# Performance work log

Measured on AMD Instinct MI355X. Metric: run time of the kernel, lower is better.

The kernel has to match this reference:

```python
import jax, jax.numpy as jnp
import numpy as np

N = 16384      # total points
B = 8          # point clouds in batch
PER = N // B   # points per cloud (batch ids sorted in blocks)
M = 4096       # sampled centers (ratio 0.25, strided sampler -> batch-aligned)
K = 64         # max_num_neighbors
R = 0.25       # ball-query radius
C_IN = 128
HID = 256
C_OUT = 256


def setup_inputs() -> dict:
    key = jax.random.key(0)
    k1, k2, k3, k4, k5 = jax.random.split(key, 5)
    x = jax.random.normal(k1, (N, C_IN), dtype=jnp.float32)
    pos = jax.random.uniform(k2, (N, 3), dtype=jnp.float32)  # unit cube
    batch = jnp.repeat(jnp.arange(B, dtype=jnp.int32), PER)  # sorted block batch ids
    lframes = jax.random.normal(k3, (N, 3, 3), dtype=jnp.float32)
    W1 = jax.random.normal(k4, (2 * C_IN + 3, HID), dtype=jnp.float32) * 0.05
    b1 = jnp.zeros((HID,), dtype=jnp.float32)
    W2 = jax.random.normal(k5, (HID, C_OUT), dtype=jnp.float32) * 0.05
    b2 = jnp.zeros((C_OUT,), dtype=jnp.float32)
    return {"x": x, "pos": pos, "batch": batch, "lframes": lframes,
            "W1": W1, "b1": b1, "W2": W2, "b2": b2}


def _ball_query(pos, batch, idx):
    """radius(pos, pos[idx], R, batch, batch[idx], max_num_neighbors=K).
    Returns fixed-size neighbor indices [M, K] + validity mask [M, K]."""
    pos_c = pos[idx]                                  # [M, 3]
    # squared distances via gemm trick (avoid [M, N, 3] broadcast)
    d2 = ((pos_c ** 2).sum(-1)[:, None]
          + (pos ** 2).sum(-1)[None, :]
          - 2.0 * pos_c @ pos.T)                      # [M, N]
    valid = (d2 <= R * R) & (batch[idx][:, None] == batch[None, :])
    score = jnp.where(valid, -d2, -jnp.inf)
    vals, nbr = jax.lax.top_k(score, K)               # K nearest within ball
    return nbr, jnp.isfinite(vals)


def reference(x, pos, batch, lframes, W1, b1, W2, b2):
    # center sampler: strided subsample (batch-aligned since batch is block-sorted)
    idx = jnp.arange(0, N, N // M)                    # [M]
    nbr, vmask = _ball_query(pos, batch, idx)         # [M, K]

    pos_dst = pos[idx]                                # [M, 3]
    x_dst = x[idx]                                    # [M, C_IN]
    lframes_dst = lframes[idx]                        # [M, 3, 3]

    # EdgeConv: per-edge message MLP([x_src, x_dst, lframe_dst @ (pos_src - pos_dst)])
    rel = pos[nbr] - pos_dst[:, None, :]              # [M, K, 3]
    rel_loc = jnp.einsum('mij,mkj->mki', lframes_dst, rel)  # rotate into dst frame
    feats = jnp.concatenate([
        x[nbr],                                        # [M, K, C_IN]
        jnp.broadcast_to(x_dst[:, None, :], (M, K, C_IN)),
        rel_loc,
    ], axis=-1)                                        # [M, K, 2*C_IN+3]

    h = jax.nn.relu(feats @ W1 + b1)                   # [M, K, HID]
    msg = h @ W2 + b2                                  # [M, K, C_OUT]

    # masked max aggregation over valid neighbors
    msg = jnp.where(vmask[..., None], msg, -jnp.inf)
    out = msg.max(axis=1)                              # [M, C_OUT]
    out = jnp.where(jnp.isfinite(out), out, 0.0)
    return out, pos_dst, batch[idx], lframes_dst
```

## Files before the change

kernel.cpp:

```cpp
#include <hip/hip_runtime.h>
#include <hip/hip_bf16.h>

#define N_PTS 16384
#define PER   2048
#define M_CTR 4096
#define KNB   64
#define C_IN  128
#define HID   256
#define C_OUT 256

typedef unsigned short u16;
typedef __attribute__((ext_vector_type(8))) short s8v;
typedef __attribute__((ext_vector_type(4))) float f4v;
typedef __attribute__((ext_vector_type(4))) unsigned int u4v;

static __device__ __forceinline__ float bf2f(u16 u) {
    union { unsigned int i; float f; } v; v.i = ((unsigned int)u) << 16; return v.f;
}
static __device__ __forceinline__ u16 f2bf(float f) {
    union { float f; unsigned int i; } v; v.f = f;
    unsigned int r = v.i + 0x7FFFu + ((v.i >> 16) & 1u);
    return (u16)(r >> 16);
}

__global__ __launch_bounds__(256) void prep_kernel(
        const float* __restrict__ W1, const float* __restrict__ W2,
        u16* __restrict__ W1aT, u16* __restrict__ W1bT, u16* __restrict__ W2T) {
    int gid = blockIdx.x * 256 + threadIdx.x;
    int c = gid >> 8, k = gid & 255;
    W2T[gid] = f2bf(W2[k * 256 + c]);
    if (gid < 32768) {
        int c1 = gid >> 7, k1 = gid & 127;
        W1aT[gid] = f2bf(W1[k1 * 256 + c1]);
        W1bT[gid] = f2bf(W1[(k1 + 128) * 256 + c1]);
    }
}

__global__ __launch_bounds__(256) void ballq_kernel(
        const float* __restrict__ pos, int* __restrict__ nbr, int* __restrict__ cnt) {
    __shared__ float cd2[1024];
    __shared__ int   cidx[1024];
    __shared__ int   s_n;
    int m = blockIdx.x, tid = threadIdx.x;
    int c = m * 4;
    int base = (m >> 9) << 11;
    if (tid == 0) s_n = 0;
    __syncthreads();
    float cx = pos[c * 3 + 0], cy = pos[c * 3 + 1], cz = pos[c * 3 + 2];
    float A = __fadd_rn(__fadd_rn(__fmul_rn(cx, cx), __fmul_rn(cy, cy)), __fmul_rn(cz, cz));
    float c2x = __fmul_rn(2.0f, cx);
    float c2y = __fmul_rn(2.0f, cy);
    float c2z = __fmul_rn(2.0f, cz);
    for (int s = 0; s < 8; ++s) {
        int j = base + tid + (s << 8);
        float px = pos[j * 3 + 0], py = pos[j * 3 + 1], pz = pos[j * 3 + 2];
        float B = __fadd_rn(__fadd_rn(__fmul_rn(px, px), __fmul_rn(py, py)), __fmul_rn(pz, pz));
        float C = __fmaf_rn(c2z, pz, __fmaf_rn(c2y, py, __fmul_rn(c2x, px)));
        float d2 = __fsub_rn(__fadd_rn(A, B), C);
        if (d2 <= 0.0625f) {
            int a = atomicAdd(&s_n, 1);
            if (a < 1024) { cd2[a] = d2; cidx[a] = j; }
        }
    }
    __syncthreads();
    int V = s_n < 1024 ? s_n : 1024;
    if (V <= KNB) {
        if (tid < KNB) nbr[m * KNB + tid] = (tid < V) ? cidx[tid] : c;
        if (tid == 0) cnt[m] = V;
    } else {
        for (int e = tid; e < V; e += 256) {
            float de = cd2[e]; int ie = cidx[e];
            int rank = 0;
            for (int q = 0; q < V; ++q) {
                float dq = cd2[q];
                rank += (dq < de) || (dq == de && cidx[q] < ie);
            }
            if (rank < KNB) nbr[m * KNB + rank] = cidx[e];
        }
        if (tid == 0) cnt[m] = KNB;
    }
}

template <int MODE>
__global__ __launch_bounds__(256) void gemm_xw_kernel(
        const float* __restrict__ x, const u16* __restrict__ WT,
        const float* __restrict__ b1, u16* __restrict__ u_out, float* __restrict__ v_out) {
    __shared__ u16 x_lds[64 * 136];
    int tid = threadIdx.x, blk = blockIdx.x;
    {
        int r = tid >> 2, q = tid & 3;
        int xrow = blk * 64 + r;
        if (MODE == 1) xrow *= 4;
        const float* xp = x + xrow * C_IN + q * 32;
        u16* dst = x_lds + r * 136 + q * 32;
        for (int i = 0; i < 8; ++i) {
            f4v f = *(const f4v*)(xp + i * 4);
            dst[i * 4 + 0] = f2bf(f[0]);
            dst[i * 4 + 1] = f2bf(f[1]);
            dst[i * 4 + 2] = f2bf(f[2]);
            dst[i * 4 + 3] = f2bf(f[3]);
        }
    }
    __syncthreads();
    int lane = tid & 63, w = tid >> 6;
    int quad = lane >> 4, l16 = lane & 15;
    int cb = w * 64;
    f4v acc[4][4] = {};
    for (int k0 = 0; k0 < 128; k0 += 32) {
        s8v a[4], b[4];
        for (int rt = 0; rt < 4; ++rt)
            a[rt] = *(const s8v*)&x_lds[(rt * 16 + l16) * 136 + k0 + quad * 8];
        for (int ct = 0; ct < 4; ++ct)
            b[ct] = *(const s8v*)(WT + (cb + ct * 16 + l16) * 128 + k0 + quad * 8);
        for (int rt = 0; rt < 4; ++rt)
            for (int ct = 0; ct < 4; ++ct)
                acc[rt][ct] = __builtin_amdgcn_mfma_f32_16x16x32_bf16(a[rt], b[ct], acc[rt][ct], 0, 0, 0);
    }
    for (int rt = 0; rt < 4; ++rt)
        for (int ct = 0; ct < 4; ++ct)
            for (int g = 0; g < 4; ++g) {
                int row = rt * 16 + quad * 4 + g;
                int col = cb + ct * 16 + l16;
                float val = acc[rt][ct][g];
                int orow = blk * 64 + row;
                if (MODE == 0) u_out[orow * 256 + col] = f2bf(val);
                else           v_out[orow * 256 + col] = val + b1[col];
            }
}

__global__ __launch_bounds__(256) void edge_kernel(
        const u16* __restrict__ u, const float* __restrict__ v,
        const u16* __restrict__ W2T, const float* __restrict__ W1,
        const float* __restrict__ b2, const float* __restrict__ pos,
        const float* __restrict__ lframes, const int* __restrict__ batch,
        const int* __restrict__ nbr, const int* __restrict__ cnt,
        float* __restrict__ out0, float* __restrict__ out_pos,
        float* __restrict__ out_batch, float* __restrict__ out_lf) {
    __shared__ u16   h_lds[64 * 264];
    __shared__ float relc_lds[64 * 4];
    __shared__ float v_lds[256];
    __shared__ float w1c_lds[768];
    __shared__ int   nbr_lds[64];
    __shared__ int   s_cnt;

    int m = blockIdx.x, tid = threadIdx.x;
    int c = m * 4;
    v_lds[tid] = v[m * 256 + tid];
    for (int i = tid; i < 768; i += 256) w1c_lds[i] = W1[65536 + i];
    if (tid == 0) s_cnt = cnt[m];
    if (tid < 64) {
        int j = nbr[m * KNB + tid];
        nbr_lds[tid] = j;
        float rx = pos[j * 3 + 0] - pos[c * 3 + 0];
        float ry = pos[j * 3 + 1] - pos[c * 3 + 1];
        float rz = pos[j * 3 + 2] - pos[c * 3 + 2];
        const float* lf = lframes + c * 9;
        relc_lds[tid * 4 + 0] = lf[0] * rx + lf[1] * ry + lf[2] * rz;
        relc_lds[tid * 4 + 1] = lf[3] * rx + lf[4] * ry + lf[5] * rz;
        relc_lds[tid * 4 + 2] = lf[6] * rx + lf[7] * ry + lf[8] * rz;
    }
    if (tid < 3)  out_pos[m * 3 + tid] = pos[c * 3 + tid];
    if (tid == 3) out_batch[m] = (float)batch[c];
    if (tid >= 4 && tid < 13) out_lf[m * 9 + (tid - 4)] = lframes[c * 9 + (tid - 4)];
    __syncthreads();

    {
        int k = tid >> 2, q = tid & 3;
        int j = nbr_lds[k];
        float r0 = relc_lds[k * 4 + 0], r1 = relc_lds[k * 4 + 1], r2 = relc_lds[k * 4 + 2];
        const u16* urow = u + j * 256 + q * 64;
        u16* hrow = h_lds + k * 264 + q * 64;
        for (int i = 0; i < 8; ++i) {
            union { u4v v4; u16 us[8]; } uu;
            uu.v4 = *(const u4v*)(urow + i * 8);
            union { u4v v4; u16 us[8]; } hh;
            for (int e = 0; e < 8; ++e) {
                int col = q * 64 + i * 8 + e;
                float pre = v_lds[col] + bf2f(uu.us[e])
                          + r0 * w1c_lds[col] + r1 * w1c_lds[256 + col] + r2 * w1c_lds[512 + col];
                hh.us[e] = f2bf(fmaxf(pre, 0.0f));
            }
            *(u4v*)(hrow + i * 8) = hh.v4;
        }
    }
    __syncthreads();

    int lane = tid & 63, w = tid >> 6;
    int quad = lane >> 4, l16 = lane & 15;
    int cb = w * 64;
    f4v acc[4][4] = {};
    for (int k0 = 0; k0 < 256; k0 += 32) {
        s8v a[4], b[4];
        for (int rt = 0; rt < 4; ++rt)
            a[rt] = *(const s8v*)&h_lds[(rt * 16 + l16) * 264 + k0 + quad * 8];
        for (int ct = 0; ct < 4; ++ct)
            b[ct] = *(const s8v*)(W2T + (cb + ct * 16 + l16) * 256 + k0 + quad * 8);
        for (int rt = 0; rt < 4; ++rt)
            for (int ct = 0; ct < 4; ++ct)
                acc[rt][ct] = __builtin_amdgcn_mfma_f32_16x16x32_bf16(a[rt], b[ct], acc[rt][ct], 0, 0, 0);
    }
    int cv = s_cnt;
    for (int ct = 0; ct < 4; ++ct) {
        float mx = -__builtin_inff();
        for (int rt = 0; rt < 4; ++rt)
            for (int g = 0; g < 4; ++g) {
                int row = rt * 16 + quad * 4 + g;
                float val = acc[rt][ct][g];
                if (row < cv) mx = fmaxf(mx, val);
            }
        mx = fmaxf(mx, __shfl_xor(mx, 16, 64));
        mx = fmaxf(mx, __shfl_xor(mx, 32, 64));
        if (lane < 16) {
            int col = cb + ct * 16 + l16;
            out0[m * 256 + col] = mx + b2[col];
        }
    }
}

extern "C" void kernel_launch(void* const* d_in, const int* in_sizes, int n_in,
                              void* d_out, int out_size, void* d_ws, size_t ws_size,
                              hipStream_t stream) {
    const float* x       = (const float*)d_in[0];
    const float* pos     = (const float*)d_in[1];
    const int*   batch   = (const int*)d_in[2];
    const float* lframes = (const float*)d_in[3];
    const float* W1      = (const float*)d_in[4];
    const float* b1      = (const float*)d_in[5];
    const float* W2      = (const float*)d_in[6];
    const float* b2      = (const float*)d_in[7];

    float* out       = (float*)d_out;
    float* out_pos   = out + M_CTR * 256;
    float* out_batch = out_pos + M_CTR * 3;
    float* out_lf    = out_batch + M_CTR;

    char* ws = (char*)d_ws;
    u16*   u_ws = (u16*)(ws);
    float* v_ws = (float*)(ws + 8388608);
    u16*   W1aT = (u16*)(ws + 12582912);
    u16*   W1bT = (u16*)(ws + 12648448);
    u16*   W2T  = (u16*)(ws + 12713984);
    int*   nbr  = (int*)(ws + 12845056);
    int*   cntp = (int*)(ws + 13893632);

    hipLaunchKernelGGL(prep_kernel, dim3(256), dim3(256), 0, stream, W1, W2, W1aT, W1bT, W2T);
    hipLaunchKernelGGL(ballq_kernel, dim3(M_CTR), dim3(256), 0, stream, pos, nbr, cntp);
    hipLaunchKernelGGL((gemm_xw_kernel<0>), dim3(N_PTS / 64), dim3(256), 0, stream,
                       x, W1aT, b1, u_ws, v_ws);
    hipLaunchKernelGGL((gemm_xw_kernel<1>), dim3(M_CTR / 64), dim3(256), 0, stream,
                       x, W1bT, b1, u_ws, v_ws);
    hipLaunchKernelGGL(edge_kernel, dim3(M_CTR), dim3(256), 0, stream,
                       u_ws, v_ws, W2T, W1, b2, pos, lframes, batch, nbr, cntp,
                       out, out_pos, out_batch, out_lf);
}
```

Before: 201.1 us.

## Merge prep into ball query, fuse both x-W1 GEMMs, and restructure edge h-construction

Folds the weight transpose/convert work into the first 256 blocks of the ball-query kernel and merges the two x@W1 GEMM launches into a single grid that picks its mode by block index, cutting the launch count from five to three. The edge kernel now keeps v and the pos-weight rows in registers instead of LDS, builds h with 32 threads per row over 8-column chunks, and packs bf16 with a truncating perm instead of rounding. It also adds a launch-bounds occupancy hint and remaps block order so consecutive blocks come from different batches. The truncating pack changes rounding slightly, and the merged GEMM grid runs uneven workloads in one launch.

```diff
diff --git a/kernel.cpp b/kernel.cpp
--- a/kernel.cpp
+++ b/kernel.cpp
@@ -10,6 +10,7 @@
 #define C_OUT 256
 
 typedef unsigned short u16;
+typedef unsigned int u32;
 typedef __attribute__((ext_vector_type(8))) short s8v;
 typedef __attribute__((ext_vector_type(4))) float f4v;
 typedef __attribute__((ext_vector_type(4))) unsigned int u4v;
@@ -23,25 +24,26 @@
     return (u16)(r >> 16);
 }
 
-__global__ __launch_bounds__(256) void prep_kernel(
+__global__ __launch_bounds__(256) void ballq_kernel(
+        const float* __restrict__ pos, int* __restrict__ nbr, int* __restrict__ cnt,
         const float* __restrict__ W1, const float* __restrict__ W2,
         u16* __restrict__ W1aT, u16* __restrict__ W1bT, u16* __restrict__ W2T) {
-    int gid = blockIdx.x * 256 + threadIdx.x;
-    int c = gid >> 8, k = gid & 255;
-    W2T[gid] = f2bf(W2[k * 256 + c]);
-    if (gid < 32768) {
-        int c1 = gid >> 7, k1 = gid & 127;
-        W1aT[gid] = f2bf(W1[k1 * 256 + c1]);
-        W1bT[gid] = f2bf(W1[(k1 + 128) * 256 + c1]);
-    }
-}
-
-__global__ __launch_bounds__(256) void ballq_kernel(
-        const float* __restrict__ pos, int* __restrict__ nbr, int* __restrict__ cnt) {
     __shared__ float cd2[1024];
     __shared__ int   cidx[1024];
     __shared__ int   s_n;
     int m = blockIdx.x, tid = threadIdx.x;
+
+    if (m < 256) {
+        int gid = m * 256 + tid;
+        int cc = gid >> 8, k = gid & 255;
+        W2T[gid] = f2bf(W2[k * 256 + cc]);
+        if (gid < 32768) {
+            int c1 = gid >> 7, k1 = gid & 127;
+            W1aT[gid] = f2bf(W1[k1 * 256 + c1]);
+            W1bT[gid] = f2bf(W1[(k1 + 128) * 256 + c1]);
+        }
+    }
+
     int c = m * 4;
     int base = (m >> 9) << 11;
     if (tid == 0) s_n = 0;
@@ -81,16 +83,18 @@
     }
 }
 
-template <int MODE>
 __global__ __launch_bounds__(256) void gemm_xw_kernel(
-        const float* __restrict__ x, const u16* __restrict__ WT,
+        const float* __restrict__ x, const u16* __restrict__ W1aT, const u16* __restrict__ W1bT,
         const float* __restrict__ b1, u16* __restrict__ u_out, float* __restrict__ v_out) {
     __shared__ u16 x_lds[64 * 136];
-    int tid = threadIdx.x, blk = blockIdx.x;
+    int blk = blockIdx.x, tid = threadIdx.x;
+    int mode = blk >= 256 ? 1 : 0;
+    int bb = mode ? blk - 256 : blk;
+    const u16* WT = mode ? W1bT : W1aT;
     {
         int r = tid >> 2, q = tid & 3;
-        int xrow = blk * 64 + r;
-        if (MODE == 1) xrow *= 4;
+        int xrow = bb * 64 + r;
+        if (mode) xrow *= 4;
         const float* xp = x + xrow * C_IN + q * 32;
         u16* dst = x_lds + r * 136 + q * 32;
         for (int i = 0; i < 8; ++i) {
@@ -122,13 +126,13 @@
                 int row = rt * 16 + quad * 4 + g;
                 int col = cb + ct * 16 + l16;
                 float val = acc[rt][ct][g];
-                int orow = blk * 64 + row;
-                if (MODE == 0) u_out[orow * 256 + col] = f2bf(val);
+                int orow = bb * 64 + row;
+                if (mode == 0) u_out[orow * 256 + col] = f2bf(val);
                 else           v_out[orow * 256 + col] = val + b1[col];
             }
 }
 
-__global__ __launch_bounds__(256) void edge_kernel(
+__global__ __launch_bounds__(256, 4) void edge_kernel(
         const u16* __restrict__ u, const float* __restrict__ v,
         const u16* __restrict__ W2T, const float* __restrict__ W1,
         const float* __restrict__ b2, const float* __restrict__ pos,
@@ -136,17 +140,15 @@
         const int* __restrict__ nbr, const int* __restrict__ cnt,
         float* __restrict__ out0, float* __restrict__ out_pos,
         float* __restrict__ out_batch, float* __restrict__ out_lf) {
-    __shared__ u16   h_lds[64 * 264];
-    __shared__ float relc_lds[64 * 4];
-    __shared__ float v_lds[256];
-    __shared__ float w1c_lds[768];
-    __shared__ int   nbr_lds[64];
-    __shared__ int   s_cnt;
-
-    int m = blockIdx.x, tid = threadIdx.x;
+    __shared__ u16 h_lds[64 * 264];
+    __shared__ f4v relc_lds[64];
+    __shared__ int nbr_lds[64];
+    __shared__ int s_cnt;
+
+    int blk = blockIdx.x, tid = threadIdx.x;
+    int m = ((blk & 7) << 9) | (blk >> 3);
     int c = m * 4;
-    v_lds[tid] = v[m * 256 + tid];
-    for (int i = tid; i < 768; i += 256) w1c_lds[i] = W1[65536 + i];
+
     if (tid == 0) s_cnt = cnt[m];
     if (tid < 64) {
         int j = nbr[m * KNB + tid];
@@ -155,33 +157,50 @@
         float ry = pos[j * 3 + 1] - pos[c * 3 + 1];
         float rz = pos[j * 3 + 2] - pos[c * 3 + 2];
         const float* lf = lframes + c * 9;
-        relc_lds[tid * 4 + 0] = lf[0] * rx + lf[1] * ry + lf[2] * rz;
-        relc_lds[tid * 4 + 1] = lf[3] * rx + lf[4] * ry + lf[5] * rz;
-        relc_lds[tid * 4 + 2] = lf[6] * rx + lf[7] * ry + lf[8] * rz;
+        f4v r;
+        r[0] = lf[0] * rx + lf[1] * ry + lf[2] * rz;
+        r[1] = lf[3] * rx + lf[4] * ry + lf[5] * rz;
+        r[2] = lf[6] * rx + lf[7] * ry + lf[8] * rz;
+        r[3] = 0.0f;
+        relc_lds[tid] = r;
     }
     if (tid < 3)  out_pos[m * 3 + tid] = pos[c * 3 + tid];
     if (tid == 3) out_batch[m] = (float)batch[c];
     if (tid >= 4 && tid < 13) out_lf[m * 9 + (tid - 4)] = lframes[c * 9 + (tid - 4)];
-    __syncthreads();
-
-    {
-        int k = tid >> 2, q = tid & 3;
+
+    int co = (tid & 31) * 8;
+    int rs = tid >> 5;
+    const float* w1c = W1 + 65536;
+    f4v vv0 = *(const f4v*)(v + m * 256 + co);
+    f4v vv1 = *(const f4v*)(v + m * 256 + co + 4);
+    f4v wa0 = *(const f4v*)(w1c + co),        wa1 = *(const f4v*)(w1c + co + 4);
+    f4v wb0 = *(const f4v*)(w1c + 256 + co),  wb1 = *(const f4v*)(w1c + 256 + co + 4);
+    f4v wc0 = *(const f4v*)(w1c + 512 + co),  wc1 = *(const f4v*)(w1c + 512 + co + 4);
+    __syncthreads();
+
+    #pragma unroll
+    for (int ii = 0; ii < 8; ++ii) {
+        int k = rs + ii * 8;
         int j = nbr_lds[k];
-        float r0 = relc_lds[k * 4 + 0], r1 = relc_lds[k * 4 + 1], r2 = relc_lds[k * 4 + 2];
-        const u16* urow = u + j * 256 + q * 64;
-        u16* hrow = h_lds + k * 264 + q * 64;
-        for (int i = 0; i < 8; ++i) {
-            union { u4v v4; u16 us[8]; } uu;
-            uu.v4 = *(const u4v*)(urow + i * 8);
-            union { u4v v4; u16 us[8]; } hh;
-            for (int e = 0; e < 8; ++e) {
-                int col = q * 64 + i * 8 + e;
-                float pre = v_lds[col] + bf2f(uu.us[e])
-                          + r0 * w1c_lds[col] + r1 * w1c_lds[256 + col] + r2 * w1c_lds[512 + col];
-                hh.us[e] = f2bf(fmaxf(pre, 0.0f));
-            }
-            *(u4v*)(hrow + i * 8) = hh.v4;
-        }
+        f4v r = relc_lds[k];
+        u4v uu = *(const u4v*)(u + j * 256 + co);
+        float p[8];
+        #pragma unroll
+        for (int e = 0; e < 8; ++e) {
+            u16 ue = (u16)((uu[e >> 1] >> ((e & 1) * 16)) & 0xFFFFu);
+            float va = (e < 4) ? vv0[e] : vv1[e - 4];
+            float a0 = (e < 4) ? wa0[e] : wa1[e - 4];
+            float b0 = (e < 4) ? wb0[e] : wb1[e - 4];
+            float c0 = (e < 4) ? wc0[e] : wc1[e - 4];
+            float pre = fmaf(r[0], a0, fmaf(r[1], b0, fmaf(r[2], c0, va + bf2f(ue))));
+            p[e] = fmaxf(pre, 0.0f);
+        }
+        u4v pk;
+        #pragma unroll
+        for (int d = 0; d < 4; ++d)
+            pk[d] = __builtin_amdgcn_perm(__float_as_uint(p[2 * d + 1]),
+                                          __float_as_uint(p[2 * d]), 0x07060302u);
+        *(u4v*)&h_lds[k * 264 + co] = pk;
     }
     __syncthreads();
 
@@ -243,12 +262,10 @@
     int*   nbr  = (int*)(ws + 12845056);
     int*   cntp = (int*)(ws + 13893632);
 
-    hipLaunchKernelGGL(prep_kernel, dim3(256), dim3(256), 0, stream, W1, W2, W1aT, W1bT, W2T);
-    hipLaunchKernelGGL(ballq_kernel, dim3(M_CTR), dim3(256), 0, stream, pos, nbr, cntp);
-    hipLaunchKernelGGL((gemm_xw_kernel<0>), dim3(N_PTS / 64), dim3(256), 0, stream,
-                       x, W1aT, b1, u_ws, v_ws);
-    hipLaunchKernelGGL((gemm_xw_kernel<1>), dim3(M_CTR / 64), dim3(256), 0, stream,
-                       x, W1bT, b1, u_ws, v_ws);
+    hipLaunchKernelGGL(ballq_kernel, dim3(M_CTR), dim3(256), 0, stream,
+                       pos, nbr, cntp, W1, W2, W1aT, W1bT, W2T);
+    hipLaunchKernelGGL(gemm_xw_kernel, dim3(320), dim3(256), 0, stream,
+                       x, W1aT, W1bT, b1, u_ws, v_ws);
     hipLaunchKernelGGL(edge_kernel, dim3(M_CTR), dim3(256), 0, stream,
                        u_ws, v_ws, W2T, W1, b2, pos, lframes, batch, nbr, cntp,
                        out, out_pos, out_batch, out_lf);
```

After: 185.1 us. -8.0%, faster.
